# Kernel optimization log

Hardware: AMD Instinct MI355X
Metric: run time of the kernel (lower is better)

## Reference

```python
import jax, jax.numpy as jnp
import numpy as np

BN_EPS = 1e-5


def _guide_net(fullres, w1, b1, bn_gamma, bn_beta, bn_mean, bn_var, w2, b2):
    # two 1x1 convs == channel matmuls
    x = jnp.einsum('nchw,oc->nohw', fullres, w1[:, :, 0, 0]) + b1[None, :, None, None]
    inv = bn_gamma / jnp.sqrt(bn_var + BN_EPS)
    x = (x - bn_mean[None, :, None, None]) * inv[None, :, None, None] + bn_beta[None, :, None, None]
    x = jax.nn.relu(x)
    g = jnp.einsum('nchw,oc->nohw', x, w2[:, :, 0, 0]) + b2[None, :, None, None]
    return jax.nn.sigmoid(g)  # [N,1,H,W] in (0,1)


def _slice_one(grid_n, guide_n):
    # grid_n: [C,D,h,w]; guide_n: [H,W]; trilinear grid_sample, align_corners=True.
    C, D, h, w = grid_n.shape
    H, W = guide_n.shape
    # normalized coords in torch code map exactly to voxel coords [0, size-1]
    gz = guide_n * (D - 1)                      # per-pixel depth coord [H,W]
    z0f = jnp.floor(gz)
    tz = (gz - z0f)[None, :, :]                 # [1,H,W]
    z0 = jnp.clip(z0f, 0, D - 1).astype(jnp.int32)
    z1 = jnp.clip(z0f + 1, 0, D - 1).astype(jnp.int32)
    gy = jnp.linspace(0.0, h - 1.0, H)
    y0f = jnp.floor(gy)
    ty = (gy - y0f)[None, :, None]              # [1,H,1]
    y0 = jnp.clip(y0f, 0, h - 1).astype(jnp.int32)[:, None]
    y1 = jnp.clip(y0f + 1, 0, h - 1).astype(jnp.int32)[:, None]
    gx = jnp.linspace(0.0, w - 1.0, W)
    x0f = jnp.floor(gx)
    tx = (gx - x0f)[None, None, :]              # [1,1,W]
    x0 = jnp.clip(x0f, 0, w - 1).astype(jnp.int32)[None, :]
    x1 = jnp.clip(x0f + 1, 0, w - 1).astype(jnp.int32)[None, :]

    def g(z, y, x):
        # z:[H,W], y:[H,1], x:[1,W] -> broadcast gather -> [C,H,W]
        return grid_n[:, z, y, x]

    def lerp_xy(z):
        a = g(z, y0, x0) * (1 - tx) + g(z, y0, x1) * tx
        b = g(z, y1, x0) * (1 - tx) + g(z, y1, x1) * tx
        return a * (1 - ty) + b * ty

    return lerp_xy(z0) * (1 - tz) + lerp_xy(z1) * tz  # [C,H,W]


def _apply_coeffs(coeff, fullres):
    # coeff: [N,12,H,W]; rows (0:3,+3), (4:7,+7), (8:11,+11)
    N, _, H, W = coeff.shape
    A = coeff[:, jnp.array([0, 1, 2, 4, 5, 6, 8, 9, 10])].reshape(N, 3, 3, H, W)
    bias = coeff[:, jnp.array([3, 7, 11])]
    return jnp.einsum('nkchw,nchw->nkhw', A, fullres) + bias


def setup_inputs() -> dict:
    key = jax.random.key(0)
    ks = jax.random.split(key, 10)
    N, H, W = 2, 1080, 1920
    return {
        'fullres': jax.random.uniform(ks[0], (N, 3, H, W), jnp.float32),
        'bilateral_grid': jax.random.normal(ks[1], (N, 12, 8, 16, 16), jnp.float32),
        'w1': jax.random.normal(ks[2], (16, 3, 1, 1), jnp.float32) * 0.2,
        'b1': jax.random.normal(ks[3], (16,), jnp.float32) * 0.1,
        'bn_gamma': jax.random.uniform(ks[4], (16,), jnp.float32, 0.5, 1.5),
        'bn_beta': jax.random.normal(ks[5], (16,), jnp.float32) * 0.1,
        'bn_mean': jax.random.normal(ks[6], (16,), jnp.float32) * 0.1,
        'bn_var': jax.random.uniform(ks[7], (16,), jnp.float32, 0.5, 1.5),
        'w2': jax.random.normal(ks[8], (1, 16, 1, 1), jnp.float32) * 0.2,
        'b2': jax.random.normal(ks[9], (1,), jnp.float32) * 0.1,
    }


def reference(fullres, bilateral_grid, w1, b1, bn_gamma, bn_beta, bn_mean, bn_var, w2, b2):
    guide = _guide_net(fullres, w1, b1, bn_gamma, bn_beta, bn_mean, bn_var, w2, b2)  # [N,1,H,W]
    coeff = jax.vmap(_slice_one)(bilateral_grid, guide[:, 0])                         # [N,12,H,W]
    return _apply_coeffs(coeff, fullres)                                              # [N,3,H,W]
```

## Files before the change

### kernel.cpp

```cpp
#include <hip/hip_runtime.h>
#include <hip/hip_bf16.h>
#include <math.h>

#define HWV (1080 * 1920)
#define NPIX (2 * HWV)

typedef _Float16 half2 __attribute__((ext_vector_type(2)));
typedef __fp16   pk2   __attribute__((ext_vector_type(2)));
union U32H2 { unsigned u; half2 h; pk2 p; };

__global__ void prep_kernel(const float* __restrict__ grid,
                            const float* __restrict__ w1,
                            const float* __restrict__ b1,
                            const float* __restrict__ gamma,
                            const float* __restrict__ beta,
                            const float* __restrict__ mean,
                            const float* __restrict__ var,
                            const float* __restrict__ w2,
                            const float* __restrict__ b2,
                            float* __restrict__ wsg,
                            float* __restrict__ wsw) {
    int i = blockIdx.x * blockDim.x + threadIdx.x;
    if (i < 2 * 12 * 8 * 16 * 16) {
        int c = i % 12;
        int t = i / 12;
        int z = t % 8;  t /= 8;
        int x = t % 16; t /= 16;
        int y = t % 16;
        int n = t / 16;
        wsg[i] = grid[n * 24576 + c * 2048 + z * 256 + y * 16 + x];
    }
    if (i < 16) {
        float inv = gamma[i] / sqrtf(var[i] + 1e-5f);
        wsw[i]      = w1[i * 3 + 0] * inv;
        wsw[16 + i] = w1[i * 3 + 1] * inv;
        wsw[32 + i] = w1[i * 3 + 2] * inv;
        wsw[48 + i] = (b1[i] - mean[i]) * inv + beta[i];
        wsw[64 + i] = w2[i];
    }
    if (i == 0) wsw[80] = b2[0];
    if (i < 8) {
        int c0 = 2 * i, c1 = 2 * i + 1;
        float inv0 = gamma[c0] / sqrtf(var[c0] + 1e-5f);
        float inv1 = gamma[c1] / sqrtf(var[c1] + 1e-5f);
        unsigned* wp = (unsigned*)(wsw + 84);
        U32H2 t;
        t.p = __builtin_amdgcn_cvt_pkrtz(w1[c0*3+0] * inv0, w1[c1*3+0] * inv1);
        wp[i * 4 + 0] = t.u;
        t.p = __builtin_amdgcn_cvt_pkrtz(w1[c0*3+1] * inv0, w1[c1*3+1] * inv1);
        wp[i * 4 + 1] = t.u;
        t.p = __builtin_amdgcn_cvt_pkrtz(w1[c0*3+2] * inv0, w1[c1*3+2] * inv1);
        wp[i * 4 + 2] = t.u;
        t.p = __builtin_amdgcn_cvt_pkrtz((b1[c0] - mean[c0]) * inv0 + beta[c0],
                                         (b1[c1] - mean[c1]) * inv1 + beta[c1]);
        wp[i * 4 + 3] = t.u;
    }
}

__global__ __launch_bounds__(512, 8) void fused_kernel(
        const float* __restrict__ fullres,
        const float* __restrict__ wsg,
        const float* __restrict__ wsw,
        float* __restrict__ out) {
    __shared__ float sg[6 * 96];

    const int tid = threadIdx.x;
    const int n   = blockIdx.z;
    const int y   = blockIdx.y;
    const int xs  = blockIdx.x * 512;
    const int x   = xs + tid;
    const bool act = (x < 1920);

    const int p  = y * 1920 + min(x, 1919);
    const float* fr = fullres + n * 3 * HWV + p;
    float r = fr[0];
    float g = fr[HWV];
    float b = fr[2 * HWV];

    const int a = (int)((float)xs * (15.0f / 1919.0f));
    {
        float gy = (float)y * (15.0f / 1079.0f);
        float y0f = floorf(gy);
        float ty = gy - y0f;
        int y0 = min((int)y0f, 15);
        int y1 = min(y0 + 1, 15);
        const float* gbase = wsg + n * 24576;
        for (int idx = tid; idx < 576; idx += 512) {
            int k = idx / 96;
            int f = idx - k * 96;
            int xc = min(a + k, 15);
            float g0 = gbase[(y0 * 16 + xc) * 96 + f];
            float g1 = gbase[(y1 * 16 + xc) * 96 + f];
            sg[idx] = fmaf(ty, g1 - g0, g0);
        }
    }
    __syncthreads();

    if (!act) return;

    U32H2 rr, gg, bb;
    rr.p = __builtin_amdgcn_cvt_pkrtz(r, r);
    gg.p = __builtin_amdgcn_cvt_pkrtz(g, g);
    bb.p = __builtin_amdgcn_cvt_pkrtz(b, b);
    const unsigned* wp = (const unsigned*)(wsw + 84);
    const half2 zero = {(_Float16)0.0f, (_Float16)0.0f};
    float acc = wsw[80];
#pragma unroll
    for (int c2 = 0; c2 < 8; ++c2) {
        U32H2 wr, wg, wb, wbs;
        wr.u  = wp[c2 * 4 + 0];
        wg.u  = wp[c2 * 4 + 1];
        wb.u  = wp[c2 * 4 + 2];
        wbs.u = wp[c2 * 4 + 3];
        half2 h = wr.h * rr.h + (wg.h * gg.h + (wb.h * bb.h + wbs.h));
        h = __builtin_elementwise_max(h, zero);
        acc = fmaf((float)h.x, wsw[64 + 2 * c2],     acc);
        acc = fmaf((float)h.y, wsw[64 + 2 * c2 + 1], acc);
    }
    float e = __expf(-acc);
    float guide = __builtin_amdgcn_rcpf(1.0f + e);

    float gz = guide * 7.0f;
    float z0f = floorf(gz);
    float tz = gz - z0f;
    int z0 = min((int)z0f, 7);
    int z1 = min(z0 + 1, 7);

    float gx = (float)x * (15.0f / 1919.0f);
    float x0f = floorf(gx);
    float tx = gx - x0f;
    int x0 = (int)x0f;
    int k0 = x0 - a;
    int k1 = min(x0 + 1, 15) - a;

    float wx0 = 1.0f - tx, wx1 = tx;
    float wz0 = 1.0f - tz, wz1 = tz;
    float w00 = wx0 * wz0, w01 = wx0 * wz1;
    float w10 = wx1 * wz0, w11 = wx1 * wz1;

    const float4* s00 = (const float4*)(sg + k0 * 96 + z0 * 12);
    const float4* s01 = (const float4*)(sg + k0 * 96 + z1 * 12);
    const float4* s10 = (const float4*)(sg + k1 * 96 + z0 * 12);
    const float4* s11 = (const float4*)(sg + k1 * 96 + z1 * 12);

    float co[12];
#pragma unroll
    for (int c = 0; c < 12; ++c) co[c] = 0.0f;

#pragma unroll
    for (int q = 0; q < 3; ++q) {
        float4 v00 = s00[q];
        float4 v01 = s01[q];
        float4 v10 = s10[q];
        float4 v11 = s11[q];
        co[q*4+0] = fmaf(w00, v00.x, fmaf(w01, v01.x, fmaf(w10, v10.x, fmaf(w11, v11.x, co[q*4+0]))));
        co[q*4+1] = fmaf(w00, v00.y, fmaf(w01, v01.y, fmaf(w10, v10.y, fmaf(w11, v11.y, co[q*4+1]))));
        co[q*4+2] = fmaf(w00, v00.z, fmaf(w01, v01.z, fmaf(w10, v10.z, fmaf(w11, v11.z, co[q*4+2]))));
        co[q*4+3] = fmaf(w00, v00.w, fmaf(w01, v01.w, fmaf(w10, v10.w, fmaf(w11, v11.w, co[q*4+3]))));
    }

    float* op = out + n * 3 * HWV + p;
    op[0]       = fmaf(co[0], r, fmaf(co[1], g, fmaf(co[2],  b, co[3])));
    op[HWV]     = fmaf(co[4], r, fmaf(co[5], g, fmaf(co[6],  b, co[7])));
    op[2 * HWV] = fmaf(co[8], r, fmaf(co[9], g, fmaf(co[10], b, co[11])));
}

extern "C" void kernel_launch(void* const* d_in, const int* in_sizes, int n_in,
                              void* d_out, int out_size, void* d_ws, size_t ws_size,
                              hipStream_t stream) {
    const float* fullres = (const float*)d_in[0];
    const float* grid    = (const float*)d_in[1];
    const float* w1      = (const float*)d_in[2];
    const float* b1      = (const float*)d_in[3];
    const float* gamma   = (const float*)d_in[4];
    const float* beta    = (const float*)d_in[5];
    const float* mean    = (const float*)d_in[6];
    const float* var     = (const float*)d_in[7];
    const float* w2      = (const float*)d_in[8];
    const float* b2      = (const float*)d_in[9];
    float* out = (float*)d_out;

    float* wsg = (float*)d_ws;
    float* wsw = wsg + 49152;

    prep_kernel<<<192, 256, 0, stream>>>(grid, w1, b1, gamma, beta, mean, var,
                                         w2, b2, wsg, wsw);

    dim3 grid_dim(4, 1080, 2);
    fused_kernel<<<grid_dim, 512, 0, stream>>>(fullres, wsg, wsw, out);
}
```

Baseline: 33.64 us.

## Store sliced grid as fp16 pairs in split LDS arrays and interpolate with packed math

The per-row shared tile of y-interpolated grid coefficients is now stored as packed fp16 pairs in two arrays (4 and 2 words per z slice), with an extra padded z slot so z1 no longer needs clamping. Trilinear interpolation over x and z uses packed half2 FMAs on these words instead of 48 fp32 FMAs over float4 LDS reads. This halves LDS traffic and ALU work for the coefficient interpolation, at the cost of fp16 rounding in the coefficients, which may hurt accuracy. The z=8 padding slot duplicates z=7 so the original clamp behavior is kept.

```diff
diff --git a/kernel.cpp b/kernel.cpp
--- a/kernel.cpp
+++ b/kernel.cpp
@@ -62,7 +62,8 @@
         const float* __restrict__ wsg,
         const float* __restrict__ wsw,
         float* __restrict__ out) {
-    __shared__ float sg[6 * 96];
+    __shared__ unsigned slo[6][9][4];
+    __shared__ unsigned shi[6][9][2];
 
     const int tid = threadIdx.x;
     const int n   = blockIdx.z;
@@ -85,13 +86,21 @@
         int y0 = min((int)y0f, 15);
         int y1 = min(y0 + 1, 15);
         const float* gbase = wsg + n * 24576;
-        for (int idx = tid; idx < 576; idx += 512) {
-            int k = idx / 96;
-            int f = idx - k * 96;
+        if (tid < 324) {
+            int k = tid / 54;
+            int rem = tid - k * 54;
+            int z = rem / 6;
+            int j = rem - z * 6;
+            int zz = min(z, 7);
             int xc = min(a + k, 15);
-            float g0 = gbase[(y0 * 16 + xc) * 96 + f];
-            float g1 = gbase[(y1 * 16 + xc) * 96 + f];
-            sg[idx] = fmaf(ty, g1 - g0, g0);
+            const float2 v0 = *(const float2*)(gbase + ((y0 * 16 + xc) * 8 + zz) * 12 + 2 * j);
+            const float2 v1 = *(const float2*)(gbase + ((y1 * 16 + xc) * 8 + zz) * 12 + 2 * j);
+            float e0 = fmaf(ty, v1.x - v0.x, v0.x);
+            float e1 = fmaf(ty, v1.y - v0.y, v0.y);
+            U32H2 t;
+            t.p = __builtin_amdgcn_cvt_pkrtz(e0, e1);
+            if (j < 4) slo[k][z][j] = t.u;
+            else       shi[k][z][j - 4] = t.u;
         }
     }
     __syncthreads();
@@ -124,7 +133,7 @@
     float z0f = floorf(gz);
     float tz = gz - z0f;
     int z0 = min((int)z0f, 7);
-    int z1 = min(z0 + 1, 7);
+    int z1 = z0 + 1;
 
     float gx = (float)x * (15.0f / 1919.0f);
     float x0f = floorf(gx);
@@ -135,34 +144,45 @@
 
     float wx0 = 1.0f - tx, wx1 = tx;
     float wz0 = 1.0f - tz, wz1 = tz;
-    float w00 = wx0 * wz0, w01 = wx0 * wz1;
-    float w10 = wx1 * wz0, w11 = wx1 * wz1;
-
-    const float4* s00 = (const float4*)(sg + k0 * 96 + z0 * 12);
-    const float4* s01 = (const float4*)(sg + k0 * 96 + z1 * 12);
-    const float4* s10 = (const float4*)(sg + k1 * 96 + z0 * 12);
-    const float4* s11 = (const float4*)(sg + k1 * 96 + z1 * 12);
-
-    float co[12];
+
+    U32H2 w00h, w01h, w10h, w11h;
+    w00h.p = __builtin_amdgcn_cvt_pkrtz(wx0 * wz0, wx0 * wz0);
+    w01h.p = __builtin_amdgcn_cvt_pkrtz(wx0 * wz1, wx0 * wz1);
+    w10h.p = __builtin_amdgcn_cvt_pkrtz(wx1 * wz0, wx1 * wz0);
+    w11h.p = __builtin_amdgcn_cvt_pkrtz(wx1 * wz1, wx1 * wz1);
+
+    const uint4 A0 = *(const uint4*)&slo[k0][z0][0];
+    const uint4 A1 = *(const uint4*)&slo[k0][z1][0];
+    const uint4 B0 = *(const uint4*)&slo[k1][z0][0];
+    const uint4 B1 = *(const uint4*)&slo[k1][z1][0];
+    const uint2 C0 = *(const uint2*)&shi[k0][z0][0];
+    const uint2 C1 = *(const uint2*)&shi[k0][z1][0];
+    const uint2 D0 = *(const uint2*)&shi[k1][z0][0];
+    const uint2 D1 = *(const uint2*)&shi[k1][z1][0];
+
+    unsigned a0j[6] = {A0.x, A0.y, A0.z, A0.w, C0.x, C0.y};
+    unsigned a1j[6] = {A1.x, A1.y, A1.z, A1.w, C1.x, C1.y};
+    unsigned b0j[6] = {B0.x, B0.y, B0.z, B0.w, D0.x, D0.y};
+    unsigned b1j[6] = {B1.x, B1.y, B1.z, B1.w, D1.x, D1.y};
+
+    half2 hc[6];
 #pragma unroll
-    for (int c = 0; c < 12; ++c) co[c] = 0.0f;
-
-#pragma unroll
-    for (int q = 0; q < 3; ++q) {
-        float4 v00 = s00[q];
-        float4 v01 = s01[q];
-        float4 v10 = s10[q];
-        float4 v11 = s11[q];
-        co[q*4+0] = fmaf(w00, v00.x, fmaf(w01, v01.x, fmaf(w10, v10.x, fmaf(w11, v11.x, co[q*4+0]))));
-        co[q*4+1] = fmaf(w00, v00.y, fmaf(w01, v01.y, fmaf(w10, v10.y, fmaf(w11, v11.y, co[q*4+1]))));
-        co[q*4+2] = fmaf(w00, v00.z, fmaf(w01, v01.z, fmaf(w10, v10.z, fmaf(w11, v11.z, co[q*4+2]))));
-        co[q*4+3] = fmaf(w00, v00.w, fmaf(w01, v01.w, fmaf(w10, v10.w, fmaf(w11, v11.w, co[q*4+3]))));
+    for (int j = 0; j < 6; ++j) {
+        U32H2 ua0, ua1, ub0, ub1;
+        ua0.u = a0j[j]; ua1.u = a1j[j]; ub0.u = b0j[j]; ub1.u = b1j[j];
+        half2 h = w00h.h * ua0.h + (w01h.h * ua1.h);
+        h = w10h.h * ub0.h + h;
+        h = w11h.h * ub1.h + h;
+        hc[j] = h;
     }
 
     float* op = out + n * 3 * HWV + p;
-    op[0]       = fmaf(co[0], r, fmaf(co[1], g, fmaf(co[2],  b, co[3])));
-    op[HWV]     = fmaf(co[4], r, fmaf(co[5], g, fmaf(co[6],  b, co[7])));
-    op[2 * HWV] = fmaf(co[8], r, fmaf(co[9], g, fmaf(co[10], b, co[11])));
+    op[0]       = fmaf((float)hc[0].x, r, fmaf((float)hc[0].y, g,
+                  fmaf((float)hc[1].x, b, (float)hc[1].y)));
+    op[HWV]     = fmaf((float)hc[2].x, r, fmaf((float)hc[2].y, g,
+                  fmaf((float)hc[3].x, b, (float)hc[3].y)));
+    op[2 * HWV] = fmaf((float)hc[4].x, r, fmaf((float)hc[4].y, g,
+                  fmaf((float)hc[5].x, b, (float)hc[5].y)));
 }
 
 extern "C" void kernel_launch(void* const* d_in, const int* in_sizes, int n_in,
```

Result: no change. 33.37 us (-0.8%).
